# Kernel tuning notes

Hardware: AMD Instinct MI355X
Metric: run time of the kernel (lower is better)

The kernel has to match this reference:

```python
import jax, jax.numpy as jnp
import numpy as np

B, T, H = 32, 2048, 512
D = 2 * H  # bidirectional encoder feature dim


def setup_inputs() -> dict:
    key = jax.random.key(0)
    k1, k2, k3, k4, k5 = jax.random.split(key, 5)
    stdv = 1.0 / np.sqrt(H)
    return {
        "hidden": jax.random.normal(k1, (B, D), dtype=jnp.float32),
        "encoder_outputs": jax.random.normal(k2, (B, T, D), dtype=jnp.float32),
        "W_attn": jax.random.normal(k3, (H, 2 * D), dtype=jnp.float32) * stdv,
        "b_attn": jax.random.normal(k4, (H,), dtype=jnp.float32) * stdv,
        "v": jax.random.normal(k5, (H,), dtype=jnp.float32) * stdv,
    }


def reference(hidden, encoder_outputs, W_attn, b_attn, v):
    # The original per-timestep sliding-window loop recomputes a position-wise
    # Linear+tanh+dot whose value is independent of the window index, and
    # overlapping writes overwrite with identical values. The exact same math
    # is full additive attention over all T positions.
    d = encoder_outputs.shape[-1]
    Wh = W_attn[:, :d]   # acts on repeated decoder hidden state
    We = W_attn[:, d:]   # acts on encoder outputs
    # [B, H] ; avoids materializing the [B, T, 4H] concat
    hid_proj = jnp.einsum('bd,hd->bh', hidden, Wh)
    # [B, T, H]
    energy = jnp.tanh(jnp.einsum('btd,hd->bth', encoder_outputs, We)
                      + hid_proj[:, None, :] + b_attn)
    scores = jnp.einsum('bth,h->bt', energy, v)  # [B, T]
    return jax.nn.softmax(scores, axis=1)[:, None, :]  # [B, 1, T]
```

## Files before the change

kernel.cpp:

```cpp
#include <hip/hip_runtime.h>

#define Bv 32
#define Tv 2048
#define Hv 512
#define Dv 1024

using bf16x8 = __attribute__((ext_vector_type(8))) __bf16;
using f32x4  = __attribute__((ext_vector_type(4))) float;

__global__ void swizzle_we(const float* __restrict__ W, bf16x8* __restrict__ We_sw) {
    int s    = blockIdx.x * 256 + threadIdx.x;
    int lane = s & 63;
    int kt   = (s >> 6) & 31;
    int nt   = s >> 11;
    int h    = nt * 16 + (lane & 15);
    int d    = kt * 32 + ((lane >> 4) << 3);
    const float* src = W + h * (2 * Dv) + Dv + d;
    float4 f0 = *(const float4*)src;
    float4 f1 = *(const float4*)(src + 4);
    bf16x8 o;
    o[0] = (__bf16)f0.x; o[1] = (__bf16)f0.y; o[2] = (__bf16)f0.z; o[3] = (__bf16)f0.w;
    o[4] = (__bf16)f1.x; o[5] = (__bf16)f1.y; o[6] = (__bf16)f1.z; o[7] = (__bf16)f1.w;
    We_sw[s] = o;
}

__global__ void hid_proj_kernel(const float* __restrict__ hidden,
                                const float* __restrict__ W,
                                const float* __restrict__ b_attn,
                                float* __restrict__ hp) {
    int h   = blockIdx.x;
    int tid = threadIdx.x;
    float4 wh = ((const float4*)(W + h * (2 * Dv)))[tid];
    __shared__ float red[4];
    int lane = tid & 63, w = tid >> 6;
    for (int b = 0; b < Bv; ++b) {
        float4 x = ((const float4*)(hidden + b * Dv))[tid];
        float p = wh.x * x.x + wh.y * x.y + wh.z * x.z + wh.w * x.w;
#pragma unroll
        for (int m = 1; m < 64; m <<= 1) p += __shfl_xor(p, m);
        if (lane == 0) red[w] = p;
        __syncthreads();
        if (tid == 0) hp[b * Hv + h] = red[0] + red[1] + red[2] + red[3] + b_attn[h];
        __syncthreads();
    }
}

__global__ __launch_bounds__(512) void attn_main(
    const float* __restrict__ enc, const bf16x8* __restrict__ Bg,
    const float* __restrict__ hp, const float* __restrict__ vvec,
    float* __restrict__ scores)
{
    __shared__ bf16x8 As8[512];
    __shared__ float  redbuf[8][64];

    const int tid  = threadIdx.x;
    const int lane = tid & 63;
    const int w    = tid >> 6;
    const int row0 = blockIdx.x * 64;
    const int batch = row0 >> 11;

    const int srow  = ((tid >> 7) << 4) + (lane & 15);
    const int skloc = (((tid >> 6) & 1) << 5) + ((lane >> 4) << 3);
    const float* gA = enc + (row0 + srow) * Dv + skloc;

    f32x4 acc[4][4];
#pragma unroll
    for (int i = 0; i < 4; ++i)
#pragma unroll
        for (int j = 0; j < 4; ++j)
            acc[i][j] = (f32x4){0.f, 0.f, 0.f, 0.f};

    float4 f0 = *(const float4*)gA;
    float4 f1 = *(const float4*)(gA + 4);

    for (int kc = 0; kc < 16; ++kc) {
        bf16x8 bfrag[2][4];
#pragma unroll
        for (int ktl = 0; ktl < 2; ++ktl)
#pragma unroll
            for (int j = 0; j < 4; ++j)
                bfrag[ktl][j] = Bg[((w * 4 + j) * 32 + (kc * 2 + ktl)) * 64 + lane];

        __syncthreads();
        bf16x8 o;
        o[0] = (__bf16)f0.x; o[1] = (__bf16)f0.y; o[2] = (__bf16)f0.z; o[3] = (__bf16)f0.w;
        o[4] = (__bf16)f1.x; o[5] = (__bf16)f1.y; o[6] = (__bf16)f1.z; o[7] = (__bf16)f1.w;
        As8[tid] = o;
        if (kc + 1 < 16) {
            f0 = *(const float4*)(gA + (kc + 1) * 64);
            f1 = *(const float4*)(gA + (kc + 1) * 64 + 4);
        }
        __syncthreads();

#pragma unroll
        for (int ktl = 0; ktl < 2; ++ktl) {
            bf16x8 a0 = As8[(0 * 2 + ktl) * 64 + lane];
            bf16x8 a1 = As8[(1 * 2 + ktl) * 64 + lane];
            bf16x8 a2 = As8[(2 * 2 + ktl) * 64 + lane];
            bf16x8 a3 = As8[(3 * 2 + ktl) * 64 + lane];
#pragma unroll
            for (int j = 0; j < 4; ++j) {
                acc[0][j] = __builtin_amdgcn_mfma_f32_16x16x32_bf16(a0, bfrag[ktl][j], acc[0][j], 0, 0, 0);
                acc[1][j] = __builtin_amdgcn_mfma_f32_16x16x32_bf16(a1, bfrag[ktl][j], acc[1][j], 0, 0, 0);
                acc[2][j] = __builtin_amdgcn_mfma_f32_16x16x32_bf16(a2, bfrag[ktl][j], acc[2][j], 0, 0, 0);
                acc[3][j] = __builtin_amdgcn_mfma_f32_16x16x32_bf16(a3, bfrag[ktl][j], acc[3][j], 0, 0, 0);
            }
        }
    }

    float hpv[4], vv[4];
#pragma unroll
    for (int j = 0; j < 4; ++j) {
        int n  = w * 64 + j * 16 + (lane & 15);
        hpv[j] = hp[batch * Hv + n];
        vv[j]  = vvec[n];
    }
    const int qrow = (lane >> 4) * 4;
#pragma unroll
    for (int mt = 0; mt < 4; ++mt)
#pragma unroll
        for (int r = 0; r < 4; ++r) {
            float p = 0.f;
#pragma unroll
            for (int j = 0; j < 4; ++j)
                p += vv[j] * tanhf(acc[mt][j][r] + hpv[j]);
            p += __shfl_xor(p, 1);
            p += __shfl_xor(p, 2);
            p += __shfl_xor(p, 4);
            p += __shfl_xor(p, 8);
            if ((lane & 15) == 0)
                redbuf[w][mt * 16 + qrow + r] = p;
        }
    __syncthreads();
    if (tid < 64) {
        float s = 0.f;
#pragma unroll
        for (int ww = 0; ww < 8; ++ww) s += redbuf[ww][tid];
        scores[row0 + tid] = s;
    }
}

__global__ void softmax_kernel(const float* __restrict__ scores, float* __restrict__ out) {
    int b   = blockIdx.x;
    int tid = threadIdx.x;
    const float* s = scores + b * Tv;
    float local[8];
    float m = -1e30f;
#pragma unroll
    for (int i = 0; i < 8; ++i) { local[i] = s[tid + i * 256]; m = fmaxf(m, local[i]); }
    __shared__ float red[4];
    int lane = tid & 63, w = tid >> 6;
#pragma unroll
    for (int x = 1; x < 64; x <<= 1) m = fmaxf(m, __shfl_xor(m, x));
    if (lane == 0) red[w] = m;
    __syncthreads();
    m = fmaxf(fmaxf(red[0], red[1]), fmaxf(red[2], red[3]));
    float sum = 0.f;
#pragma unroll
    for (int i = 0; i < 8; ++i) { local[i] = expf(local[i] - m); sum += local[i]; }
#pragma unroll
    for (int x = 1; x < 64; x <<= 1) sum += __shfl_xor(sum, x);
    __syncthreads();
    if (lane == 0) red[w] = sum;
    __syncthreads();
    sum = red[0] + red[1] + red[2] + red[3];
    float inv = 1.0f / sum;
#pragma unroll
    for (int i = 0; i < 8; ++i) out[b * Tv + tid + i * 256] = local[i] * inv;
}

extern "C" void kernel_launch(void* const* d_in, const int* in_sizes, int n_in,
                              void* d_out, int out_size, void* d_ws, size_t ws_size,
                              hipStream_t stream) {
    const float* hidden = (const float*)d_in[0];
    const float* enc    = (const float*)d_in[1];
    const float* W      = (const float*)d_in[2];
    const float* b_attn = (const float*)d_in[3];
    const float* v      = (const float*)d_in[4];
    float* out = (float*)d_out;

    char* ws = (char*)d_ws;
    bf16x8* We_sw = (bf16x8*)ws;
    float*  hp    = (float*)(ws + (1 << 20));
    float*  sc    = (float*)(ws + (1 << 20) + (1 << 16));

    swizzle_we<<<256, 256, 0, stream>>>(W, We_sw);
    hid_proj_kernel<<<Hv, 256, 0, stream>>>(hidden, W, b_attn, hp);
    attn_main<<<(Bv * Tv) / 64, 512, 0, stream>>>(enc, We_sw, hp, v, sc);
    softmax_kernel<<<Bv, 256, 0, stream>>>(sc, out);
}
```

Before: 468.7 us.

## Double-buffer A tile in LDS, prefetch B fragments, use fast tanh

The main GEMM kernel now double-buffers the encoder tile in padded LDS, which removes one barrier per k-step, and prefetches the next iteration's weight fragments into registers. Global reads of the encoder rows become row-contiguous and coalesced. The swizzle kernel now reads W coalesced and scatters its writes. The hidden projection kernel batches its reductions behind a single barrier. tanhf is replaced by an exp-based fast tanh, which trades some accuracy and adds register pressure from the prefetched B fragments.

```diff
diff --git a/kernel.cpp b/kernel.cpp
--- a/kernel.cpp
+++ b/kernel.cpp
@@ -6,21 +6,20 @@
 #define Dv 1024
 
 using bf16x8 = __attribute__((ext_vector_type(8))) __bf16;
+using bf16x4 = __attribute__((ext_vector_type(4))) __bf16;
 using f32x4  = __attribute__((ext_vector_type(4))) float;
 
 __global__ void swizzle_we(const float* __restrict__ W, bf16x8* __restrict__ We_sw) {
-    int s    = blockIdx.x * 256 + threadIdx.x;
-    int lane = s & 63;
-    int kt   = (s >> 6) & 31;
-    int nt   = s >> 11;
-    int h    = nt * 16 + (lane & 15);
-    int d    = kt * 32 + ((lane >> 4) << 3);
+    int g = blockIdx.x * 256 + threadIdx.x;
+    int h = g >> 7;
+    int d = (g & 127) * 8;
     const float* src = W + h * (2 * Dv) + Dv + d;
     float4 f0 = *(const float4*)src;
     float4 f1 = *(const float4*)(src + 4);
     bf16x8 o;
     o[0] = (__bf16)f0.x; o[1] = (__bf16)f0.y; o[2] = (__bf16)f0.z; o[3] = (__bf16)f0.w;
     o[4] = (__bf16)f1.x; o[5] = (__bf16)f1.y; o[6] = (__bf16)f1.z; o[7] = (__bf16)f1.w;
+    int s = ((h >> 4) * 32 + (d >> 5)) * 64 + (((d >> 3) & 3) << 4) + (h & 15);
     We_sw[s] = o;
 }
 
@@ -31,18 +30,24 @@
     int h   = blockIdx.x;
     int tid = threadIdx.x;
     float4 wh = ((const float4*)(W + h * (2 * Dv)))[tid];
-    __shared__ float red[4];
+    __shared__ float red[4][Bv];
     int lane = tid & 63, w = tid >> 6;
     for (int b = 0; b < Bv; ++b) {
         float4 x = ((const float4*)(hidden + b * Dv))[tid];
         float p = wh.x * x.x + wh.y * x.y + wh.z * x.z + wh.w * x.w;
 #pragma unroll
         for (int m = 1; m < 64; m <<= 1) p += __shfl_xor(p, m);
-        if (lane == 0) red[w] = p;
-        __syncthreads();
-        if (tid == 0) hp[b * Hv + h] = red[0] + red[1] + red[2] + red[3] + b_attn[h];
-        __syncthreads();
-    }
+        if (lane == 0) red[w][b] = p;
+    }
+    __syncthreads();
+    if (tid < Bv)
+        hp[tid * Hv + h] = red[0][tid] + red[1][tid] + red[2][tid] + red[3][tid] + b_attn[h];
+}
+
+__device__ __forceinline__ float fast_tanh(float x) {
+    float xc = fminf(fmaxf(x, -9.0f), 9.0f);
+    float e  = __expf(2.0f * xc);
+    return 1.0f - 2.0f / (e + 1.0f);
 }
 
 __global__ __launch_bounds__(512) void attn_main(
@@ -50,18 +55,21 @@
     const float* __restrict__ hp, const float* __restrict__ vvec,
     float* __restrict__ scores)
 {
-    __shared__ bf16x8 As8[512];
-    __shared__ float  redbuf[8][64];
-
-    const int tid  = threadIdx.x;
-    const int lane = tid & 63;
-    const int w    = tid >> 6;
-    const int row0 = blockIdx.x * 64;
+    __shared__ __align__(16) __bf16 Abuf[2][64 * 72];
+    __shared__ float redbuf[8][64];
+
+    const int tid   = threadIdx.x;
+    const int lane  = tid & 63;
+    const int w     = tid >> 6;
+    const int row0  = blockIdx.x * 64;
     const int batch = row0 >> 11;
 
-    const int srow  = ((tid >> 7) << 4) + (lane & 15);
-    const int skloc = (((tid >> 6) & 1) << 5) + ((lane >> 4) << 3);
-    const float* gA = enc + (row0 + srow) * Dv + skloc;
+    const int srow = tid >> 3;
+    const int sd0  = (tid & 7) * 4;
+    const float* gA = enc + (row0 + srow) * Dv + sd0;
+    __bf16* lw0 = &Abuf[0][srow * 72 + sd0];
+
+    const bf16x8* Bptr = Bg + (w * 4 * 32) * 64 + lane;
 
     f32x4 acc[4][4];
 #pragma unroll
@@ -71,41 +79,59 @@
             acc[i][j] = (f32x4){0.f, 0.f, 0.f, 0.f};
 
     float4 f0 = *(const float4*)gA;
-    float4 f1 = *(const float4*)(gA + 4);
+    float4 f1 = *(const float4*)(gA + 32);
+    bf16x8 Bc[2][4];
+#pragma unroll
+    for (int ktl = 0; ktl < 2; ++ktl)
+#pragma unroll
+        for (int j = 0; j < 4; ++j)
+            Bc[ktl][j] = Bptr[(j * 32 + ktl) * 64];
+
+    const int arow  = lane & 15;
+    const int acol8 = (lane >> 4) * 8;
 
     for (int kc = 0; kc < 16; ++kc) {
-        bf16x8 bfrag[2][4];
+        __bf16* p = lw0 + (kc & 1) * (64 * 72);
+        bf16x4 o0, o1;
+        o0[0] = (__bf16)f0.x; o0[1] = (__bf16)f0.y; o0[2] = (__bf16)f0.z; o0[3] = (__bf16)f0.w;
+        o1[0] = (__bf16)f1.x; o1[1] = (__bf16)f1.y; o1[2] = (__bf16)f1.z; o1[3] = (__bf16)f1.w;
+        *(bf16x4*)p        = o0;
+        *(bf16x4*)(p + 32) = o1;
+        if (kc < 15) {
+            f0 = *(const float4*)(gA + (kc + 1) * 64);
+            f1 = *(const float4*)(gA + (kc + 1) * 64 + 32);
+        }
+        __syncthreads();
+
+        bf16x8 Bn[2][4];
+        if (kc < 15) {
+#pragma unroll
+            for (int ktl = 0; ktl < 2; ++ktl)
+#pragma unroll
+                for (int j = 0; j < 4; ++j)
+                    Bn[ktl][j] = Bptr[(j * 32 + (kc + 1) * 2 + ktl) * 64];
+        }
+
+        const __bf16* rb = &Abuf[kc & 1][0];
+#pragma unroll
+        for (int ktl = 0; ktl < 2; ++ktl) {
+            bf16x8 a0 = *(const bf16x8*)(rb + (0 * 16 + arow) * 72 + ktl * 32 + acol8);
+            bf16x8 a1 = *(const bf16x8*)(rb + (1 * 16 + arow) * 72 + ktl * 32 + acol8);
+            bf16x8 a2 = *(const bf16x8*)(rb + (2 * 16 + arow) * 72 + ktl * 32 + acol8);
+            bf16x8 a3 = *(const bf16x8*)(rb + (3 * 16 + arow) * 72 + ktl * 32 + acol8);
+#pragma unroll
+            for (int j = 0; j < 4; ++j) {
+                acc[0][j] = __builtin_amdgcn_mfma_f32_16x16x32_bf16(a0, Bc[ktl][j], acc[0][j], 0, 0, 0);
+                acc[1][j] = __builtin_amdgcn_mfma_f32_16x16x32_bf16(a1, Bc[ktl][j], acc[1][j], 0, 0, 0);
+                acc[2][j] = __builtin_amdgcn_mfma_f32_16x16x32_bf16(a2, Bc[ktl][j], acc[2][j], 0, 0, 0);
+                acc[3][j] = __builtin_amdgcn_mfma_f32_16x16x32_bf16(a3, Bc[ktl][j], acc[3][j], 0, 0, 0);
+            }
+        }
 #pragma unroll
         for (int ktl = 0; ktl < 2; ++ktl)
 #pragma unroll
             for (int j = 0; j < 4; ++j)
-                bfrag[ktl][j] = Bg[((w * 4 + j) * 32 + (kc * 2 + ktl)) * 64 + lane];
-
-        __syncthreads();
-        bf16x8 o;
-        o[0] = (__bf16)f0.x; o[1] = (__bf16)f0.y; o[2] = (__bf16)f0.z; o[3] = (__bf16)f0.w;
-        o[4] = (__bf16)f1.x; o[5] = (__bf16)f1.y; o[6] = (__bf16)f1.z; o[7] = (__bf16)f1.w;
-        As8[tid] = o;
-        if (kc + 1 < 16) {
-            f0 = *(const float4*)(gA + (kc + 1) * 64);
-            f1 = *(const float4*)(gA + (kc + 1) * 64 + 4);
-        }
-        __syncthreads();
-
-#pragma unroll
-        for (int ktl = 0; ktl < 2; ++ktl) {
-            bf16x8 a0 = As8[(0 * 2 + ktl) * 64 + lane];
-            bf16x8 a1 = As8[(1 * 2 + ktl) * 64 + lane];
-            bf16x8 a2 = As8[(2 * 2 + ktl) * 64 + lane];
-            bf16x8 a3 = As8[(3 * 2 + ktl) * 64 + lane];
-#pragma unroll
-            for (int j = 0; j < 4; ++j) {
-                acc[0][j] = __builtin_amdgcn_mfma_f32_16x16x32_bf16(a0, bfrag[ktl][j], acc[0][j], 0, 0, 0);
-                acc[1][j] = __builtin_amdgcn_mfma_f32_16x16x32_bf16(a1, bfrag[ktl][j], acc[1][j], 0, 0, 0);
-                acc[2][j] = __builtin_amdgcn_mfma_f32_16x16x32_bf16(a2, bfrag[ktl][j], acc[2][j], 0, 0, 0);
-                acc[3][j] = __builtin_amdgcn_mfma_f32_16x16x32_bf16(a3, bfrag[ktl][j], acc[3][j], 0, 0, 0);
-            }
-        }
+                Bc[ktl][j] = Bn[ktl][j];
     }
 
     float hpv[4], vv[4];
@@ -123,7 +149,7 @@
             float p = 0.f;
 #pragma unroll
             for (int j = 0; j < 4; ++j)
-                p += vv[j] * tanhf(acc[mt][j][r] + hpv[j]);
+                p += vv[j] * fast_tanh(acc[mt][j][r] + hpv[j]);
             p += __shfl_xor(p, 1);
             p += __shfl_xor(p, 2);
             p += __shfl_xor(p, 4);
```

New measurement: 443.2 us. -5.4%, faster.
